# Optimization experiments

Measured on AMD Instinct MI355X. Metric: run time of the kernel, lower is better.

## Reference

```python
import jax, jax.numpy as jnp
import numpy as np

D_MODEL = 1024
N_HEADS = 16
DEPTH = D_MODEL // N_HEADS
P_FEAT = 64
NEG_BIG = -1.0e9


def setup_inputs() -> dict:
    key = jax.random.key(0)
    ks = jax.random.split(key, 12)
    B, S = 4, 2048
    s = 1.0 / np.sqrt(D_MODEL)
    return {
        "q": jax.random.normal(ks[0], (B, S, D_MODEL), jnp.float32),
        "k": jax.random.normal(ks[1], (B, S, D_MODEL), jnp.float32),
        "v": jax.random.normal(ks[2], (B, S, D_MODEL), jnp.float32),
        "protocol_features": jax.random.normal(ks[3], (B, P_FEAT), jnp.float32),
        "mask": jax.random.randint(ks[4], (B, 1, 1, S), 0, 2).astype(jnp.float32),
        "wq": jax.random.normal(ks[5], (D_MODEL, D_MODEL), jnp.float32) * s,
        "bq": jnp.zeros((D_MODEL,), jnp.float32),
        "wk": jax.random.normal(ks[6], (D_MODEL, D_MODEL), jnp.float32) * s,
        "bk": jnp.zeros((D_MODEL,), jnp.float32),
        "wv": jax.random.normal(ks[7], (D_MODEL, D_MODEL), jnp.float32) * s,
        "bv": jnp.zeros((D_MODEL,), jnp.float32),
        "wg": jax.random.normal(ks[8], (P_FEAT, N_HEADS), jnp.float32) * (1.0 / np.sqrt(P_FEAT)),
        "bg": jnp.zeros((N_HEADS,), jnp.float32),
    }


def _split_heads(x, B):
    # [B,S,d_model] -> [B,H,S,depth]
    return x.reshape(B, -1, N_HEADS, DEPTH).transpose(0, 2, 1, 3)


def reference(q, k, v, protocol_features, mask, wq, bq, wk, bk, wv, bv, wg, bg):
    B = q.shape[0]
    qh = _split_heads(q @ wq + bq, B)
    kh = _split_heads(k @ wk + bk, B)
    vh = _split_heads(v @ wv + bv, B)
    # scaled QK^T: [B,H,S,S]
    logits = jnp.einsum("bhqd,bhkd->bhqk", qh, kh) / jnp.sqrt(jnp.float32(DEPTH))
    # per-head protocol gate (sigmoid), broadcast over q/k positions
    validity = jax.nn.sigmoid(protocol_features @ wg + bg)  # [B,H]
    logits = logits * validity[:, :, None, None]
    logits = logits + mask * NEG_BIG
    attn = jax.nn.softmax(logits, axis=-1)
    out = jnp.einsum("bhqk,bhkd->bhqd", attn, vh)
    concat = out.transpose(0, 2, 1, 3).reshape(B, -1, D_MODEL)
    return concat, attn
```

## Files before the change

### kernel.cpp

```cpp
#include <hip/hip_runtime.h>

#define S_LEN 2048
#define NB 4
#define NH 16
#define BHN 64
#define DM 1024
#define DEP 64
#define MROWS 8192

typedef __attribute__((ext_vector_type(8))) short short8;
typedef __attribute__((ext_vector_type(4))) short s16x4;
typedef __attribute__((ext_vector_type(4))) float f32x4;

#define MFMA_BF16(a, b, c) __builtin_amdgcn_mfma_f32_16x16x32_bf16((a), (b), (c), 0, 0, 0)

__device__ __forceinline__ void mfma16(const s16x4& a, const s16x4& b, f32x4& c) {
  asm("v_mfma_f32_16x16x16_bf16 %0, %1, %2, %0" : "+v"(c) : "v"(a), "v"(b));
}

typedef __attribute__((address_space(1))) const void* as1cv;
typedef __attribute__((address_space(3))) void* as3v;

__device__ __forceinline__ void gld16(const void* g, void* l) {
  __builtin_amdgcn_global_load_lds((as1cv)g, (as3v)l, 16, 0, 0);
}

__device__ __forceinline__ unsigned short f2bf(float f) {
  unsigned u = __float_as_uint(f);
  u += 0x7fffu + ((u >> 16) & 1u);
  return (unsigned short)(u >> 16);
}

__device__ __forceinline__ unsigned cvtpk(float a, float b) {
  unsigned r;
  asm("v_cvt_pk_bf16_f32 %0, %1, %2" : "=v"(r) : "v"(a), "v"(b));
  return r;
}

__device__ __forceinline__ int SWZ(int row, int gran) {
  return row * 64 + ((gran ^ (row & 7)) << 3);
}

__global__ void gate_kernel(const float* __restrict__ pf, const float* __restrict__ wg,
                            const float* __restrict__ bg, float* __restrict__ validity) {
  int t = threadIdx.x;
  int b = t >> 4, h = t & 15;
  float s = bg[h];
  for (int i = 0; i < 64; i++) s += pf[b * 64 + i] * wg[i * NH + h];
  validity[t] = 1.0f / (1.0f + __expf(-s));
}

__global__ __launch_bounds__(256) void wt3_kernel(const float* __restrict__ wq,
                                                  const float* __restrict__ wk,
                                                  const float* __restrict__ wv,
                                                  unsigned short* __restrict__ WtBase) {
  __shared__ unsigned short T[64][72];
  int z = blockIdx.z;
  const float* W = (z == 0) ? wq : (z == 1) ? wk : wv;
  unsigned short* Wt = WtBase + (size_t)z * DM * DM;
  int k0 = blockIdx.x * 64, n0 = blockIdx.y * 64;
  int t = threadIdx.x;
  int r = t >> 2, c4 = (t & 3) * 16;
  for (int j = 0; j < 16; j += 4) {
    float4 v = *(const float4*)&W[(size_t)(k0 + r) * DM + n0 + c4 + j];
    T[r][c4 + j + 0] = f2bf(v.x); T[r][c4 + j + 1] = f2bf(v.y);
    T[r][c4 + j + 2] = f2bf(v.z); T[r][c4 + j + 3] = f2bf(v.w);
  }
  __syncthreads();
  union { unsigned short us[16]; uint4 v[2]; } o;
  for (int j = 0; j < 16; j++) o.us[j] = T[c4 + j][r];
  *(uint4*)&Wt[(size_t)(n0 + r) * DM + k0 + c4] = o.v[0];
  *(uint4*)&Wt[(size_t)(n0 + r) * DM + k0 + c4 + 8] = o.v[1];
}

__global__ __launch_bounds__(256) void proj3_gemm(const float* __restrict__ Xq,
                                                  const float* __restrict__ Xk,
                                                  const float* __restrict__ Xv,
                                                  const unsigned short* __restrict__ BtBase,
                                                  const float* __restrict__ bq,
                                                  const float* __restrict__ bk,
                                                  const float* __restrict__ bv,
                                                  unsigned short* __restrict__ Ybase,
                                                  unsigned short* __restrict__ vhT) {
  __shared__ union {
    struct { unsigned short As[128 * 64]; unsigned short Bs[128 * 64]; } s;
    unsigned short T[128 * 130];
  } u;
  const int K = DM;
  int z = blockIdx.z;
  const float* X = (z == 0) ? Xq : (z == 1) ? Xk : Xv;
  const float* bias = (z == 0) ? bq : (z == 1) ? bk : bv;
  const unsigned short* Bt = BtBase + (size_t)z * DM * DM;
  unsigned short* Y = Ybase + (size_t)z * MROWS * DM;
  unsigned short* As = u.s.As;
  unsigned short* Bs = u.s.Bs;

  int tid = threadIdx.x, w = tid >> 6, l = tid & 63, g = l >> 4, lc = l & 15;
  int r0 = blockIdx.x * 128, c0 = blockIdx.y * 128;
  int wr = w >> 1, wc = w & 1;
  int lrow = l >> 3, lcol = (l & 7) * 8;
  int sr = tid >> 3, sc = (tid & 7) * 8;
  f32x4 acc[4][4] = {};
  for (int k0 = 0; k0 < K; k0 += 64) {
    __syncthreads();
    for (int i = 0; i < 4; i++) {
      int row = (w * 4 + i) * 8 + lrow;
      gld16(Bt + (size_t)(c0 + row) * K + k0 + lcol, &Bs[(w * 4 + i) * 512]);
    }
    for (int i = 0; i < 4; i++) {
      int row = i * 32 + sr;
      const float* src = X + (size_t)(r0 + row) * K + k0 + sc;
      float4 a0 = *(const float4*)src;
      float4 a1 = *(const float4*)(src + 4);
      uint4 o = {cvtpk(a0.x, a0.y), cvtpk(a0.z, a0.w),
                 cvtpk(a1.x, a1.y), cvtpk(a1.z, a1.w)};
      *(uint4*)&As[row * 64 + sc] = o;
    }
    __syncthreads();
    for (int kk = 0; kk < 2; kk++) {
      short8 a[4], b[4];
      for (int m = 0; m < 4; m++)
        a[m] = *(const short8*)&As[(wr * 64 + m * 16 + lc) * 64 + kk * 32 + g * 8];
      for (int n = 0; n < 4; n++)
        b[n] = *(const short8*)&Bs[(wc * 64 + n * 16 + lc) * 64 + kk * 32 + g * 8];
      for (int m = 0; m < 4; m++)
        for (int n = 0; n < 4; n++)
          acc[m][n] = MFMA_BF16(a[m], b[n], acc[m][n]);
    }
  }
  if (z < 2) {
    for (int n = 0; n < 4; n++) {
      int c = c0 + wc * 64 + n * 16 + lc;
      float bi = bias[c];
      int h = c >> 6, d = c & 63;
      for (int m = 0; m < 4; m++) {
        int rowbase = r0 + wr * 64 + m * 16 + g * 4;
        for (int r = 0; r < 4; r++) {
          int row = rowbase + r;
          int b_ = row >> 11, s = row & 2047;
          Y[(((size_t)b_ * NH + h) * S_LEN + s) * DEP + d] = f2bf(acc[m][n][r] + bi);
        }
      }
    }
  } else {
    __syncthreads();
    for (int n = 0; n < 4; n++) {
      int dl = wc * 64 + n * 16 + lc;
      float bi = bias[c0 + dl];
      for (int m = 0; m < 4; m++) {
        int sl = wr * 64 + m * 16 + g * 4;
        uint2 pk;
        pk.x = cvtpk(acc[m][n][0] + bi, acc[m][n][1] + bi);
        pk.y = cvtpk(acc[m][n][2] + bi, acc[m][n][3] + bi);
        *(uint2*)&u.T[dl * 130 + sl] = pk;
      }
    }
    __syncthreads();
    int b_ = r0 >> 11, s0 = r0 & 2047;
    int dl0 = tid >> 4, seg = tid & 15;
    for (int i = 0; i < 8; i++) {
      int dl = dl0 + i * 16;
      int c = c0 + dl;
      int h = c >> 6, dd = c & 63;
      unsigned short* dst =
          vhT + (((size_t)b_ * NH + h) * DEP + dd) * S_LEN + s0 + seg * 8;
      *(uint4*)dst = *(const uint4*)&u.T[dl * 130 + seg * 8];
    }
  }
}

__global__ __launch_bounds__(512) void attn_fused(const unsigned short* __restrict__ qh,
                                                  const unsigned short* __restrict__ kh,
                                                  const unsigned short* __restrict__ vhT,
                                                  const float* __restrict__ validity,
                                                  const float* __restrict__ mask,
                                                  float* __restrict__ concat,
                                                  float* __restrict__ attn) {
  __shared__ unsigned short Qs[128 * 64];
  __shared__ unsigned short KV[4][64 * 64];
  __shared__ unsigned short MsB[S_LEN];

  int id = blockIdx.x;
  int cxcd = id & 7, j = id >> 3;
  int bh = cxcd * 8 + (j >> 4);
  int q0 = (j & 15) * 128;
  int b = bh >> 4, h = bh & 15;

  int tid = threadIdx.x, w = tid >> 6, l = tid & 63, g = l >> 4, lc = l & 15;
  int srow = l >> 3;
  int sgran = (l & 7) ^ srow;
  float scale = validity[bh] * 0.125f * 1.44269504f;
  for (int i = tid; i < S_LEN; i += 512)
    MsB[i] = f2bf(mask[(size_t)b * S_LEN + i] * (-1.44269504e9f));

  const unsigned short* qb = qh + (size_t)bh * S_LEN * DEP;
  const unsigned short* kb = kh + (size_t)bh * S_LEN * DEP;
  const unsigned short* vb = vhT + (size_t)bh * DEP * S_LEN;
  int qrow = w * 16 + lc;

  unsigned short* B0 = &KV[0][0];
  unsigned short* B1 = &KV[2][0];
  for (int i = 0; i < 2; i++)
    gld16(qb + (size_t)(q0 + i * 64 + w * 8 + srow) * DEP + sgran * 8,
          &Qs[(i * 64 + w * 8) * 64]);
  for (int i = 0; i < 2; i++)
    gld16(kb + (size_t)(i * 64 + w * 8 + srow) * DEP + sgran * 8,
          B0 + (i * 64 + w * 8) * 64);
  __syncthreads();
  short8 aq0 = *(const short8*)&Qs[SWZ(qrow, g)];
  short8 aq1 = *(const short8*)&Qs[SWZ(qrow, 4 + g)];

  float ell = 0.f;
  for (int kt2 = 0; kt2 < 16; kt2++) {
    const int cb = kt2 & 1;
    unsigned short* cur = cb ? B1 : B0;
    if (kt2 < 15) {
      unsigned short* nxt = cb ? B0 : B1;
      for (int i = 0; i < 2; i++)
        gld16(kb + (size_t)((kt2 + 1) * 128 + i * 64 + w * 8 + srow) * DEP + sgran * 8,
              nxt + (i * 64 + w * 8) * 64);
    }
    for (int f = 0; f < 8; f++) {
      int krow = f * 16 + lc;
      short8 ak0 = *(const short8*)&cur[SWZ(krow, g)];
      short8 ak1 = *(const short8*)&cur[SWZ(krow, 4 + g)];
      f32x4 c = {};
      __builtin_amdgcn_s_setprio(1);
      c = MFMA_BF16(ak0, aq0, c);
      c = MFMA_BF16(ak1, aq1, c);
      __builtin_amdgcn_s_setprio(0);
      uint2 mu = *(const uint2*)&MsB[kt2 * 128 + f * 16 + g * 4];
      float mb0 = __uint_as_float(mu.x << 16);
      float mb1 = __uint_as_float(mu.x & 0xFFFF0000u);
      float mb2 = __uint_as_float(mu.y << 16);
      float mb3 = __uint_as_float(mu.y & 0xFFFF0000u);
      ell += exp2f(fmaf(c[0], scale, mb0)) + exp2f(fmaf(c[1], scale, mb1)) +
             exp2f(fmaf(c[2], scale, mb2)) + exp2f(fmaf(c[3], scale, mb3));
    }
    __builtin_amdgcn_sched_barrier(0);
    asm volatile("s_waitcnt vmcnt(0)" ::: "memory");
    __builtin_amdgcn_sched_barrier(0);
    __builtin_amdgcn_s_barrier();
  }
  ell += __shfl_xor(ell, 16, 64);
  ell += __shfl_xor(ell, 32, 64);
  float rinv = 1.0f / ell;

  gld16(kb + (size_t)(w * 8 + srow) * DEP + sgran * 8, &KV[0][w * 512]);
  gld16(vb + (size_t)(w * 8 + srow) * S_LEN + sgran * 8, &KV[2][w * 512]);
  __syncthreads();

  float* arow = attn + ((size_t)bh * S_LEN + q0 + w * 16 + lc) * S_LEN + g * 4;

  f32x4 O[4] = {};
#pragma unroll 2
  for (int kt = 0; kt < 32; kt++) {
    const int cb = kt & 1;
    if (kt < 31) {
      gld16(kb + (size_t)((kt + 1) * 64 + w * 8 + srow) * DEP + sgran * 8,
            &KV[cb ^ 1][w * 512]);
      gld16(vb + (size_t)(w * 8 + srow) * S_LEN + (kt + 1) * 64 + sgran * 8,
            &KV[2 + (cb ^ 1)][w * 512]);
    }
    s16x4 pa[4];
#pragma unroll
    for (int f = 0; f < 4; f++) {
      int krow = f * 16 + lc;
      short8 ak0 = *(const short8*)&KV[cb][SWZ(krow, g)];
      short8 ak1 = *(const short8*)&KV[cb][SWZ(krow, 4 + g)];
      f32x4 c = {};
      __builtin_amdgcn_s_setprio(1);
      c = MFMA_BF16(ak0, aq0, c);
      c = MFMA_BF16(ak1, aq1, c);
      __builtin_amdgcn_s_setprio(0);
      uint2 mu = *(const uint2*)&MsB[kt * 64 + f * 16 + g * 4];
      float mb0 = __uint_as_float(mu.x << 16);
      float mb1 = __uint_as_float(mu.x & 0xFFFF0000u);
      float mb2 = __uint_as_float(mu.y << 16);
      float mb3 = __uint_as_float(mu.y & 0xFFFF0000u);
      float p0 = exp2f(fmaf(c[0], scale, mb0)) * rinv;
      float p1 = exp2f(fmaf(c[1], scale, mb1)) * rinv;
      float p2 = exp2f(fmaf(c[2], scale, mb2)) * rinv;
      float p3 = exp2f(fmaf(c[3], scale, mb3)) * rinv;
      *(f32x4*)(arow + kt * 64 + f * 16) = f32x4{p0, p1, p2, p3};
      union { unsigned u[2]; s16x4 s; } pk;
      pk.u[0] = cvtpk(p0, p1);
      pk.u[1] = cvtpk(p2, p3);
      pa[f] = pk.s;
    }
    __builtin_amdgcn_s_setprio(1);
#pragma unroll
    for (int f = 0; f < 4; f++) {
#pragma unroll
      for (int n = 0; n < 4; n++) {
        int vrow = n * 16 + lc;
        int gran = (f * 2 + (g >> 1)) ^ (vrow & 7);
        s16x4 bv = *(const s16x4*)&KV[2 + cb][vrow * 64 + gran * 8 + (g & 1) * 4];
        mfma16(pa[f], bv, O[n]);
      }
    }
    __builtin_amdgcn_s_setprio(0);
    __builtin_amdgcn_sched_barrier(0);
    if (kt < 31) { asm volatile("s_waitcnt vmcnt(4)" ::: "memory"); }
    __builtin_amdgcn_sched_barrier(0);
    __builtin_amdgcn_s_barrier();
  }
  for (int n = 0; n < 4; n++)
    for (int r = 0; r < 4; r++)
      concat[((size_t)b * S_LEN + q0 + w * 16 + g * 4 + r) * DM + h * DEP + n * 16 + lc] =
          O[n][r];
}

extern "C" void kernel_launch(void* const* d_in, const int* in_sizes, int n_in,
                              void* d_out, int out_size, void* d_ws, size_t ws_size,
                              hipStream_t stream) {
  const float* q    = (const float*)d_in[0];
  const float* k    = (const float*)d_in[1];
  const float* v    = (const float*)d_in[2];
  const float* pf   = (const float*)d_in[3];
  const float* mask = (const float*)d_in[4];
  const float* wq   = (const float*)d_in[5];
  const float* bq   = (const float*)d_in[6];
  const float* wk   = (const float*)d_in[7];
  const float* bk   = (const float*)d_in[8];
  const float* wv   = (const float*)d_in[9];
  const float* bv   = (const float*)d_in[10];
  const float* wg   = (const float*)d_in[11];
  const float* bg   = (const float*)d_in[12];

  float* concat = (float*)d_out;
  float* attn   = concat + (size_t)NB * S_LEN * DM;

  unsigned short* wqT = (unsigned short*)attn;
  unsigned short* wkT = wqT + (size_t)DM * DM;
  unsigned short* wvT = wkT + (size_t)DM * DM;

  float* validity = (float*)d_ws;
  unsigned short* qhp = (unsigned short*)((char*)d_ws + 4096);
  unsigned short* khp = qhp + (size_t)MROWS * DM;
  unsigned short* vhp = khp + (size_t)MROWS * DM;
  unsigned short* vhT = vhp + (size_t)MROWS * DM;

  gate_kernel<<<1, 64, 0, stream>>>(pf, wg, bg, validity);

  wt3_kernel<<<dim3(16, 16, 3), 256, 0, stream>>>(wq, wk, wv, wqT);

  proj3_gemm<<<dim3(64, 8, 3), 256, 0, stream>>>(q, k, v, wqT, bq, bk, bv, qhp, vhT);

  attn_fused<<<1024, 512, 0, stream>>>(qhp, khp, vhT, validity, mask, concat, attn);
}
```

Baseline: 443.8 us.

## Fuse gate into weight transpose, stage Q/K stores via LDS, use fp32 mask

The gate sigmoid computation moves into an extra z-slice of the weight-transpose kernel, which removes one kernel launch. The Q/K projection epilogue now goes through the shared-memory transpose buffer and writes 16-byte vectors instead of scattered 2-byte stores. The attention mask is kept in LDS as fp32 rather than bf16, so each read is a single vector load with no unpacking. The fp32 mask doubles the mask's LDS footprint, and the extra z-slice launches 256 blocks of which only one does any work.

```diff
diff --git a/kernel.cpp b/kernel.cpp
--- a/kernel.cpp
+++ b/kernel.cpp
@@ -7,6 +7,7 @@
 #define DM 1024
 #define DEP 64
 #define MROWS 8192
+#define NEGB (-1.44269504e9f)
 
 typedef __attribute__((ext_vector_type(8))) short short8;
 typedef __attribute__((ext_vector_type(4))) short s16x4;
@@ -41,21 +42,26 @@
   return row * 64 + ((gran ^ (row & 7)) << 3);
 }
 
-__global__ void gate_kernel(const float* __restrict__ pf, const float* __restrict__ wg,
-                            const float* __restrict__ bg, float* __restrict__ validity) {
-  int t = threadIdx.x;
-  int b = t >> 4, h = t & 15;
-  float s = bg[h];
-  for (int i = 0; i < 64; i++) s += pf[b * 64 + i] * wg[i * NH + h];
-  validity[t] = 1.0f / (1.0f + __expf(-s));
-}
-
 __global__ __launch_bounds__(256) void wt3_kernel(const float* __restrict__ wq,
                                                   const float* __restrict__ wk,
                                                   const float* __restrict__ wv,
-                                                  unsigned short* __restrict__ WtBase) {
+                                                  unsigned short* __restrict__ WtBase,
+                                                  const float* __restrict__ pf,
+                                                  const float* __restrict__ wg,
+                                                  const float* __restrict__ bg,
+                                                  float* __restrict__ validity) {
+  int z = blockIdx.z;
+  if (z == 3) {
+    if (blockIdx.x == 0 && blockIdx.y == 0 && threadIdx.x < 64) {
+      int t = threadIdx.x;
+      int b = t >> 4, h = t & 15;
+      float s = bg[h];
+      for (int i = 0; i < 64; i++) s += pf[b * 64 + i] * wg[i * NH + h];
+      validity[t] = 1.0f / (1.0f + __expf(-s));
+    }
+    return;
+  }
   __shared__ unsigned short T[64][72];
-  int z = blockIdx.z;
   const float* W = (z == 0) ? wq : (z == 1) ? wk : wv;
   unsigned short* Wt = WtBase + (size_t)z * DM * DM;
   int k0 = blockIdx.x * 64, n0 = blockIdx.y * 64;
@@ -128,35 +134,36 @@
           acc[m][n] = MFMA_BF16(a[m], b[n], acc[m][n]);
     }
   }
+  __syncthreads();
+  for (int n = 0; n < 4; n++) {
+    int dl = wc * 64 + n * 16 + lc;
+    float bi = bias[c0 + dl];
+    for (int m = 0; m < 4; m++) {
+      int sl = wr * 64 + m * 16 + g * 4;
+      uint2 pk;
+      pk.x = cvtpk(acc[m][n][0] + bi, acc[m][n][1] + bi);
+      pk.y = cvtpk(acc[m][n][2] + bi, acc[m][n][3] + bi);
+      *(uint2*)&u.T[dl * 130 + sl] = pk;
+    }
+  }
+  __syncthreads();
+  int b_ = r0 >> 11, s0 = r0 & 2047;
   if (z < 2) {
-    for (int n = 0; n < 4; n++) {
-      int c = c0 + wc * 64 + n * 16 + lc;
-      float bi = bias[c];
-      int h = c >> 6, d = c & 63;
-      for (int m = 0; m < 4; m++) {
-        int rowbase = r0 + wr * 64 + m * 16 + g * 4;
-        for (int r = 0; r < 4; r++) {
-          int row = rowbase + r;
-          int b_ = row >> 11, s = row & 2047;
-          Y[(((size_t)b_ * NH + h) * S_LEN + s) * DEP + d] = f2bf(acc[m][n][r] + bi);
-        }
+    for (int hh = 0; hh < 2; hh++) {
+      int c = c0 + hh * 64;
+      int h = c >> 6;
+      unsigned short* base = Y + (((size_t)b_ * NH + h) * S_LEN + s0) * DEP;
+      for (int p = 0; p < 4; p++) {
+        int flat = p * 2048 + tid * 8;
+        int sl = flat >> 6;
+        int d0 = flat & 63;
+        union { unsigned short us[8]; uint4 v; } o;
+        for (int jj = 0; jj < 8; jj++)
+          o.us[jj] = u.T[(hh * 64 + d0 + jj) * 130 + sl];
+        *(uint4*)(base + sl * DEP + d0) = o.v;
       }
     }
   } else {
-    __syncthreads();
-    for (int n = 0; n < 4; n++) {
-      int dl = wc * 64 + n * 16 + lc;
-      float bi = bias[c0 + dl];
-      for (int m = 0; m < 4; m++) {
-        int sl = wr * 64 + m * 16 + g * 4;
-        uint2 pk;
-        pk.x = cvtpk(acc[m][n][0] + bi, acc[m][n][1] + bi);
-        pk.y = cvtpk(acc[m][n][2] + bi, acc[m][n][3] + bi);
-        *(uint2*)&u.T[dl * 130 + sl] = pk;
-      }
-    }
-    __syncthreads();
-    int b_ = r0 >> 11, s0 = r0 & 2047;
     int dl0 = tid >> 4, seg = tid & 15;
     for (int i = 0; i < 8; i++) {
       int dl = dl0 + i * 16;
@@ -178,7 +185,7 @@
                                                   float* __restrict__ attn) {
   __shared__ unsigned short Qs[128 * 64];
   __shared__ unsigned short KV[4][64 * 64];
-  __shared__ unsigned short MsB[S_LEN];
+  __shared__ float Msf[S_LEN];
 
   int id = blockIdx.x;
   int cxcd = id & 7, j = id >> 3;
@@ -191,7 +198,7 @@
   int sgran = (l & 7) ^ srow;
   float scale = validity[bh] * 0.125f * 1.44269504f;
   for (int i = tid; i < S_LEN; i += 512)
-    MsB[i] = f2bf(mask[(size_t)b * S_LEN + i] * (-1.44269504e9f));
+    Msf[i] = mask[(size_t)b * S_LEN + i] * NEGB;
 
   const unsigned short* qb = qh + (size_t)bh * S_LEN * DEP;
   const unsigned short* kb = kh + (size_t)bh * S_LEN * DEP;
@@ -229,13 +236,9 @@
       c = MFMA_BF16(ak0, aq0, c);
       c = MFMA_BF16(ak1, aq1, c);
       __builtin_amdgcn_s_setprio(0);
-      uint2 mu = *(const uint2*)&MsB[kt2 * 128 + f * 16 + g * 4];
-      float mb0 = __uint_as_float(mu.x << 16);
-      float mb1 = __uint_as_float(mu.x & 0xFFFF0000u);
-      float mb2 = __uint_as_float(mu.y << 16);
-      float mb3 = __uint_as_float(mu.y & 0xFFFF0000u);
-      ell += exp2f(fmaf(c[0], scale, mb0)) + exp2f(fmaf(c[1], scale, mb1)) +
-             exp2f(fmaf(c[2], scale, mb2)) + exp2f(fmaf(c[3], scale, mb3));
+      f32x4 mb = *(const f32x4*)&Msf[kt2 * 128 + f * 16 + g * 4];
+      ell += exp2f(fmaf(c[0], scale, mb[0])) + exp2f(fmaf(c[1], scale, mb[1])) +
+             exp2f(fmaf(c[2], scale, mb[2])) + exp2f(fmaf(c[3], scale, mb[3]));
     }
     __builtin_amdgcn_sched_barrier(0);
     asm volatile("s_waitcnt vmcnt(0)" ::: "memory");
@@ -273,15 +276,11 @@
       c = MFMA_BF16(ak0, aq0, c);
       c = MFMA_BF16(ak1, aq1, c);
       __builtin_amdgcn_s_setprio(0);
-      uint2 mu = *(const uint2*)&MsB[kt * 64 + f * 16 + g * 4];
-      float mb0 = __uint_as_float(mu.x << 16);
-      float mb1 = __uint_as_float(mu.x & 0xFFFF0000u);
-      float mb2 = __uint_as_float(mu.y << 16);
-      float mb3 = __uint_as_float(mu.y & 0xFFFF0000u);
-      float p0 = exp2f(fmaf(c[0], scale, mb0)) * rinv;
-      float p1 = exp2f(fmaf(c[1], scale, mb1)) * rinv;
-      float p2 = exp2f(fmaf(c[2], scale, mb2)) * rinv;
-      float p3 = exp2f(fmaf(c[3], scale, mb3)) * rinv;
+      f32x4 mb = *(const f32x4*)&Msf[kt * 64 + f * 16 + g * 4];
+      float p0 = exp2f(fmaf(c[0], scale, mb[0])) * rinv;
+      float p1 = exp2f(fmaf(c[1], scale, mb[1])) * rinv;
+      float p2 = exp2f(fmaf(c[2], scale, mb[2])) * rinv;
+      float p3 = exp2f(fmaf(c[3], scale, mb[3])) * rinv;
       *(f32x4*)(arow + kt * 64 + f * 16) = f32x4{p0, p1, p2, p3};
       union { unsigned u[2]; s16x4 s; } pk;
       pk.u[0] = cvtpk(p0, p1);
@@ -334,6 +333,7 @@
   unsigned short* wqT = (unsigned short*)attn;
   unsigned short* wkT = wqT + (size_t)DM * DM;
   unsigned short* wvT = wkT + (size_t)DM * DM;
+  (void)wkT; (void)wvT;
 
   float* validity = (float*)d_ws;
   unsigned short* qhp = (unsigned short*)((char*)d_ws + 4096);
@@ -341,9 +341,7 @@
   unsigned short* vhp = khp + (size_t)MROWS * DM;
   unsigned short* vhT = vhp + (size_t)MROWS * DM;
 
-  gate_kernel<<<1, 64, 0, stream>>>(pf, wg, bg, validity);
-
-  wt3_kernel<<<dim3(16, 16, 3), 256, 0, stream>>>(wq, wk, wv, wqT);
+  wt3_kernel<<<dim3(16, 16, 4), 256, 0, stream>>>(wq, wk, wv, wqT, pf, wg, bg, validity);
 
   proj3_gemm<<<dim3(64, 8, 3), 256, 0, stream>>>(q, k, v, wqT, bq, bk, bv, qhp, vhT);
 
```

New measurement: 472.7 us. +6.5%, slower.
